# Kernel optimization log

Measured on AMD Instinct MI355X. Metric: run time of the kernel, lower is better.

The kernel has to match this reference:

```python
import jax, jax.numpy as jnp
import numpy as np

B, M, D, C = 512, 4096, 64, 256  # batch, memory_size, content_dim, controller_dim
NUM_SHIFTS = 3
EPS = 1e-8


def setup_inputs() -> dict:
    key = jax.random.key(0)
    ks = jax.random.split(key, 12)
    glorot = jax.nn.initializers.glorot_uniform()
    prev = jax.random.uniform(ks[2], (B, M), dtype=jnp.float32)
    prev = prev / jnp.sum(prev, axis=-1, keepdims=True)  # valid distribution
    return {
        "memory": jax.random.normal(ks[0], (B, M, D), dtype=jnp.float32),
        "controller_state": jax.random.normal(ks[1], (B, C), dtype=jnp.float32),
        "previous_weights": prev,
        "Wk": glorot(ks[3], (C, D), jnp.float32),
        "Wb": glorot(ks[4], (C, 1), jnp.float32),
        "bb": jnp.zeros((1,), jnp.float32),
        "Wgate": glorot(ks[5], (C, 1), jnp.float32),
        "bgate": jnp.zeros((1,), jnp.float32),
        "Ws": glorot(ks[6], (C, NUM_SHIFTS), jnp.float32),
        "bs": jnp.zeros((NUM_SHIFTS,), jnp.float32),
        "Wg": glorot(ks[7], (C, 1), jnp.float32),
        "bg": jnp.full((1,), 1.0, jnp.float32),  # sharpening_bias = 1.0
    }


def _forward(memory, controller_state, previous_weights,
             Wk, Wb, bb, Wgate, bgate, Ws, bs, Wg, bg):
    # Content addressing
    query = controller_state @ Wk                                   # (B, D)
    beta = jax.nn.softplus(controller_state @ Wb + bb) + 1.0        # (B, 1)
    qn = query / (jnp.linalg.norm(query, axis=-1, keepdims=True) + EPS)
    kn = memory / (jnp.linalg.norm(memory, axis=-1, keepdims=True) + EPS)
    sim = jnp.einsum("bd,bmd->bm", qn, kn)                          # (B, M)
    content_w = jax.nn.softmax(beta * sim, axis=-1)
    # Interpolation gate
    gate = jax.nn.sigmoid(controller_state @ Wgate + bgate)         # (B, 1)
    gated = gate * content_w + (1.0 - gate) * previous_weights
    # Location addressing: circular convolution over num_shifts
    shift_kernel = jax.nn.softmax(controller_state @ Ws + bs, axis=-1)  # (B, S)
    half = NUM_SHIFTS // 2
    shifted = jnp.zeros_like(gated)
    for i in range(NUM_SHIFTS):
        shifted = shifted + jnp.roll(gated, shift=-(i - half), axis=-1) * shift_kernel[:, i:i + 1]
    # Sharpening
    gamma = jax.nn.softplus(controller_state @ Wg + bg) + 1.0       # (B, 1)
    sharp = jnp.power(shifted + EPS, gamma)
    return sharp / (jnp.sum(sharp, axis=-1, keepdims=True) + EPS)


def reference(memory, controller_state, previous_weights,
              Wk, Wb, bb, Wgate, bgate, Ws, bs, Wg, bg):
    return _forward(memory, controller_state, previous_weights,
                    Wk, Wb, bb, Wgate, bgate, Ws, bs, Wg, bg)
```

## Files before the change

### kernel.cpp

```cpp
#include <hip/hip_runtime.h>
#include <math.h>

#define BB 512
#define MM 4096
#define DD 64
#define CC 256
#define EPS 1e-8f

__device__ __forceinline__ float softplusf(float x) {
    return (x > 20.0f) ? x : log1pf(expf(x));
}

__global__ __launch_bounds__(256) void ntm_head_kernel(
    const float* __restrict__ mem,
    const float* __restrict__ cs,
    const float* __restrict__ prev,
    const float* __restrict__ Wk,
    const float* __restrict__ Wb,
    const float* __restrict__ bb,
    const float* __restrict__ Wgate,
    const float* __restrict__ bgate,
    const float* __restrict__ Ws,
    const float* __restrict__ bs,
    const float* __restrict__ Wg,
    const float* __restrict__ bg,
    float* __restrict__ out)
{
    __shared__ float s_cs[CC];
    __shared__ __align__(16) float s_qn[DD];
    __shared__ float s_scal[8];
    __shared__ float s_logit[6];
    __shared__ float red[256];
    __shared__ float s_g[MM];

    const int tid  = threadIdx.x;
    const int b    = blockIdx.x;
    const int lane = tid & 63;
    const int wave = tid >> 6;

    s_cs[tid] = cs[b * CC + tid];
    __syncthreads();

    {
        const int d = tid & 63;
        const int part = tid >> 6;
        const int c0 = part * 64;
        float acc = 0.0f;
        #pragma unroll 8
        for (int c = 0; c < 64; ++c)
            acc = fmaf(s_cs[c0 + c], Wk[(c0 + c) * DD + d], acc);
        red[tid] = acc;
    }
    if (wave < 3) {
        const int j0 = wave * 2;
        float a0 = 0.0f, a1 = 0.0f;
        for (int c = lane; c < CC; c += 64) {
            float x = s_cs[c];
            float w0, w1;
            if (j0 == 0)      { w0 = Wb[c];       w1 = Wgate[c];    }
            else if (j0 == 2) { w0 = Ws[c * 3];   w1 = Ws[c * 3 + 1]; }
            else              { w0 = Ws[c * 3 + 2]; w1 = Wg[c];     }
            a0 = fmaf(x, w0, a0);
            a1 = fmaf(x, w1, a1);
        }
        #pragma unroll
        for (int o = 32; o > 0; o >>= 1) {
            a0 += __shfl_down(a0, o);
            a1 += __shfl_down(a1, o);
        }
        if (lane == 0) { s_logit[j0] = a0; s_logit[j0 + 1] = a1; }
    }
    __syncthreads();

    if (tid < 64) {
        float q = red[tid] + red[64 + tid] + red[128 + tid] + red[192 + tid];
        s_qn[tid] = q;
        float n = q * q;
        #pragma unroll
        for (int o = 32; o > 0; o >>= 1) n += __shfl_down(n, o);
        if (tid == 0) {
            s_scal[6] = 1.0f / (sqrtf(n) + EPS);
            float beta = softplusf(s_logit[0] + bb[0]) + 1.0f;
            float gate = 1.0f / (1.0f + expf(-(s_logit[1] + bgate[0])));
            float l0 = s_logit[2] + bs[0];
            float l1 = s_logit[3] + bs[1];
            float l2 = s_logit[4] + bs[2];
            float mx = fmaxf(l0, fmaxf(l1, l2));
            float e0 = expf(l0 - mx), e1 = expf(l1 - mx), e2 = expf(l2 - mx);
            float inv_es = 1.0f / (e0 + e1 + e2);
            float gamma = softplusf(s_logit[5] + bg[0]) + 1.0f;
            s_scal[0] = beta; s_scal[1] = gate;
            s_scal[2] = e0 * inv_es; s_scal[3] = e1 * inv_es; s_scal[4] = e2 * inv_es;
            s_scal[5] = gamma;
        }
    }
    __syncthreads();
    if (tid < 64) s_qn[tid] *= s_scal[6];
    __syncthreads();

    const float beta = s_scal[0], gate = s_scal[1];
    const float sk0 = s_scal[2], sk1 = s_scal[3], sk2 = s_scal[4];
    const float gamma = s_scal[5];
    const float4* qn4 = (const float4*)s_qn;

    float sv[16];
    float lmax = -INFINITY;
    const float* mbase = mem + (size_t)b * MM * DD;
    for (int k = 0; k < 16; ++k) {
        const int m = tid + k * 256;
        const float4* row = (const float4*)(mbase + (size_t)m * DD);
        float dot = 0.0f, nrm = 0.0f;
        #pragma unroll
        for (int d = 0; d < 16; ++d) {
            float4 v = row[d];
            float4 q = qn4[d];
            dot = fmaf(v.x, q.x, dot); dot = fmaf(v.y, q.y, dot);
            dot = fmaf(v.z, q.z, dot); dot = fmaf(v.w, q.w, dot);
            nrm = fmaf(v.x, v.x, nrm); nrm = fmaf(v.y, v.y, nrm);
            nrm = fmaf(v.z, v.z, nrm); nrm = fmaf(v.w, v.w, nrm);
        }
        float s = beta * dot / (sqrtf(nrm) + EPS);
        sv[k] = s;
        lmax = fmaxf(lmax, s);
    }

    red[tid] = lmax; __syncthreads();
    for (int o = 128; o > 0; o >>= 1) {
        if (tid < o) red[tid] = fmaxf(red[tid], red[tid + o]);
        __syncthreads();
    }
    const float mx = red[0];
    __syncthreads();
    float lsum = 0.0f;
    for (int k = 0; k < 16; ++k) { float e = expf(sv[k] - mx); sv[k] = e; lsum += e; }
    red[tid] = lsum; __syncthreads();
    for (int o = 128; o > 0; o >>= 1) {
        if (tid < o) red[tid] += red[tid + o];
        __syncthreads();
    }
    const float inv_sum = 1.0f / red[0];
    __syncthreads();

    const float* prow = prev + (size_t)b * MM;
    for (int k = 0; k < 16; ++k) {
        const int m = tid + k * 256;
        float cw = sv[k] * inv_sum;
        s_g[m] = gate * cw + (1.0f - gate) * prow[m];
    }
    __syncthreads();

    float psum = 0.0f;
    for (int k = 0; k < 16; ++k) {
        const int m = tid + k * 256;
        const int ml = (m == 0) ? (MM - 1) : (m - 1);
        const int mr = (m == MM - 1) ? 0 : (m + 1);
        float sh = s_g[ml] * sk0 + s_g[m] * sk1 + s_g[mr] * sk2;
        float p = powf(sh + EPS, gamma);
        sv[k] = p;
        psum += p;
    }
    red[tid] = psum; __syncthreads();
    for (int o = 128; o > 0; o >>= 1) {
        if (tid < o) red[tid] += red[tid + o];
        __syncthreads();
    }
    const float inv_total = 1.0f / (red[0] + EPS);

    float* orow = out + (size_t)b * MM;
    for (int k = 0; k < 16; ++k) {
        const int m = tid + k * 256;
        orow[m] = sv[k] * inv_total;
    }
}

extern "C" void kernel_launch(void* const* d_in, const int* in_sizes, int n_in,
                              void* d_out, int out_size, void* d_ws, size_t ws_size,
                              hipStream_t stream) {
    ntm_head_kernel<<<dim3(BB), dim3(256), 0, stream>>>(
        (const float*)d_in[0],
        (const float*)d_in[1],
        (const float*)d_in[2],
        (const float*)d_in[3],
        (const float*)d_in[4],
        (const float*)d_in[5],
        (const float*)d_in[6],
        (const float*)d_in[7],
        (const float*)d_in[8],
        (const float*)d_in[9],
        (const float*)d_in[10],
        (const float*)d_in[11],
        (float*)d_out);
}
```

Before: 743.8 us.

## Coalesce memory row reads with 16-lane cooperative dot products and 512 threads

Restructures the content-similarity pass so 16 lanes jointly read one memory row with float4 loads and reduce dot and norm via xor shuffles, writing scores into shared memory. Block size grows from 256 to 512 threads, and the later softmax, gating, shift and sharpening stages are remapped to 8 elements per thread. This targets the strided, uncoalesced per-thread row reads of the previous layout, at the cost of extra shuffle instructions and a shared-memory round trip for scores.

```diff
diff --git a/kernel.cpp b/kernel.cpp
--- a/kernel.cpp
+++ b/kernel.cpp
@@ -5,13 +5,14 @@
 #define MM 4096
 #define DD 64
 #define CC 256
+#define THREADS 512
 #define EPS 1e-8f
 
 __device__ __forceinline__ float softplusf(float x) {
     return (x > 20.0f) ? x : log1pf(expf(x));
 }
 
-__global__ __launch_bounds__(256) void ntm_head_kernel(
+__global__ __launch_bounds__(THREADS) void ntm_head_kernel(
     const float* __restrict__ mem,
     const float* __restrict__ cs,
     const float* __restrict__ prev,
@@ -30,18 +31,18 @@
     __shared__ __align__(16) float s_qn[DD];
     __shared__ float s_scal[8];
     __shared__ float s_logit[6];
-    __shared__ float red[256];
-    __shared__ float s_g[MM];
+    __shared__ float red[THREADS];
+    __shared__ float s_w[MM];
 
     const int tid  = threadIdx.x;
     const int b    = blockIdx.x;
     const int lane = tid & 63;
     const int wave = tid >> 6;
 
-    s_cs[tid] = cs[b * CC + tid];
-    __syncthreads();
-
-    {
+    if (tid < CC) s_cs[tid] = cs[b * CC + tid];
+    __syncthreads();
+
+    if (tid < 256) {
         const int d = tid & 63;
         const int part = tid >> 6;
         const int c0 = part * 64;
@@ -57,9 +58,9 @@
         for (int c = lane; c < CC; c += 64) {
             float x = s_cs[c];
             float w0, w1;
-            if (j0 == 0)      { w0 = Wb[c];       w1 = Wgate[c];    }
-            else if (j0 == 2) { w0 = Ws[c * 3];   w1 = Ws[c * 3 + 1]; }
-            else              { w0 = Ws[c * 3 + 2]; w1 = Wg[c];     }
+            if (j0 == 0)      { w0 = Wb[c];         w1 = Wgate[c];      }
+            else if (j0 == 2) { w0 = Ws[c * 3];     w1 = Ws[c * 3 + 1]; }
+            else              { w0 = Ws[c * 3 + 2]; w1 = Wg[c];         }
             a0 = fmaf(x, w0, a0);
             a1 = fmaf(x, w1, a1);
         }
@@ -101,40 +102,55 @@
     const float beta = s_scal[0], gate = s_scal[1];
     const float sk0 = s_scal[2], sk1 = s_scal[3], sk2 = s_scal[4];
     const float gamma = s_scal[5];
-    const float4* qn4 = (const float4*)s_qn;
-
-    float sv[16];
+
+    {
+        const int sub = lane & 15;
+        const int r   = lane >> 4;
+        const float4 q4 = ((const float4*)s_qn)[sub];
+        const float* mbase = mem + (size_t)b * MM * DD;
+        const int m0 = wave * 512 + r;
+        #pragma unroll 4
+        for (int t = 0; t < 128; ++t) {
+            const int m = m0 + t * 4;
+            const float4 v = *(const float4*)(mbase + (size_t)m * DD + sub * 4);
+            float dot = v.x * q4.x;
+            dot = fmaf(v.y, q4.y, dot);
+            dot = fmaf(v.z, q4.z, dot);
+            dot = fmaf(v.w, q4.w, dot);
+            float nrm = v.x * v.x;
+            nrm = fmaf(v.y, v.y, nrm);
+            nrm = fmaf(v.z, v.z, nrm);
+            nrm = fmaf(v.w, v.w, nrm);
+            #pragma unroll
+            for (int msk = 1; msk < 16; msk <<= 1) {
+                dot += __shfl_xor(dot, msk);
+                nrm += __shfl_xor(nrm, msk);
+            }
+            if (sub == 0)
+                s_w[m] = beta * dot / (sqrtf(nrm) + EPS);
+        }
+    }
+    __syncthreads();
+
+    float v[8];
     float lmax = -INFINITY;
-    const float* mbase = mem + (size_t)b * MM * DD;
-    for (int k = 0; k < 16; ++k) {
-        const int m = tid + k * 256;
-        const float4* row = (const float4*)(mbase + (size_t)m * DD);
-        float dot = 0.0f, nrm = 0.0f;
-        #pragma unroll
-        for (int d = 0; d < 16; ++d) {
-            float4 v = row[d];
-            float4 q = qn4[d];
-            dot = fmaf(v.x, q.x, dot); dot = fmaf(v.y, q.y, dot);
-            dot = fmaf(v.z, q.z, dot); dot = fmaf(v.w, q.w, dot);
-            nrm = fmaf(v.x, v.x, nrm); nrm = fmaf(v.y, v.y, nrm);
-            nrm = fmaf(v.z, v.z, nrm); nrm = fmaf(v.w, v.w, nrm);
-        }
-        float s = beta * dot / (sqrtf(nrm) + EPS);
-        sv[k] = s;
-        lmax = fmaxf(lmax, s);
-    }
-
+    #pragma unroll
+    for (int k = 0; k < 8; ++k) {
+        v[k] = s_w[tid + k * THREADS];
+        lmax = fmaxf(lmax, v[k]);
+    }
     red[tid] = lmax; __syncthreads();
-    for (int o = 128; o > 0; o >>= 1) {
+    for (int o = THREADS / 2; o > 0; o >>= 1) {
         if (tid < o) red[tid] = fmaxf(red[tid], red[tid + o]);
         __syncthreads();
     }
     const float mx = red[0];
     __syncthreads();
     float lsum = 0.0f;
-    for (int k = 0; k < 16; ++k) { float e = expf(sv[k] - mx); sv[k] = e; lsum += e; }
+    #pragma unroll
+    for (int k = 0; k < 8; ++k) { float e = expf(v[k] - mx); v[k] = e; lsum += e; }
     red[tid] = lsum; __syncthreads();
-    for (int o = 128; o > 0; o >>= 1) {
+    for (int o = THREADS / 2; o > 0; o >>= 1) {
         if (tid < o) red[tid] += red[tid + o];
         __syncthreads();
     }
@@ -142,41 +158,43 @@
     __syncthreads();
 
     const float* prow = prev + (size_t)b * MM;
-    for (int k = 0; k < 16; ++k) {
-        const int m = tid + k * 256;
-        float cw = sv[k] * inv_sum;
-        s_g[m] = gate * cw + (1.0f - gate) * prow[m];
+    #pragma unroll
+    for (int k = 0; k < 8; ++k) {
+        const int m = tid + k * THREADS;
+        s_w[m] = gate * (v[k] * inv_sum) + (1.0f - gate) * prow[m];
     }
     __syncthreads();
 
     float psum = 0.0f;
-    for (int k = 0; k < 16; ++k) {
-        const int m = tid + k * 256;
+    #pragma unroll
+    for (int k = 0; k < 8; ++k) {
+        const int m = tid + k * THREADS;
         const int ml = (m == 0) ? (MM - 1) : (m - 1);
         const int mr = (m == MM - 1) ? 0 : (m + 1);
-        float sh = s_g[ml] * sk0 + s_g[m] * sk1 + s_g[mr] * sk2;
+        float sh = s_w[ml] * sk0 + s_w[m] * sk1 + s_w[mr] * sk2;
         float p = powf(sh + EPS, gamma);
-        sv[k] = p;
+        v[k] = p;
         psum += p;
     }
     red[tid] = psum; __syncthreads();
-    for (int o = 128; o > 0; o >>= 1) {
+    for (int o = THREADS / 2; o > 0; o >>= 1) {
         if (tid < o) red[tid] += red[tid + o];
         __syncthreads();
     }
     const float inv_total = 1.0f / (red[0] + EPS);
 
     float* orow = out + (size_t)b * MM;
-    for (int k = 0; k < 16; ++k) {
-        const int m = tid + k * 256;
-        orow[m] = sv[k] * inv_total;
+    #pragma unroll
+    for (int k = 0; k < 8; ++k) {
+        const int m = tid + k * THREADS;
+        orow[m] = v[k] * inv_total;
     }
 }
 
 extern "C" void kernel_launch(void* const* d_in, const int* in_sizes, int n_in,
                               void* d_out, int out_size, void* d_ws, size_t ws_size,
                               hipStream_t stream) {
-    ntm_head_kernel<<<dim3(BB), dim3(256), 0, stream>>>(
+    ntm_head_kernel<<<dim3(BB), dim3(THREADS), 0, stream>>>(
         (const float*)d_in[0],
         (const float*)d_in[1],
         (const float*)d_in[2],
```

Result: faster. 727.6 us (-2.2%).
